# Performance work log

Hardware: AMD Instinct MI355X
Metric: run time of the kernel (lower is better)

## Reference

```python
import jax, jax.numpy as jnp
import numpy as np

D_MODEL = 256
NUM_HEADS = 8
DEPTH = D_MODEL // NUM_HEADS
NEG_BIG = -1e9


def setup_inputs() -> dict:
    key = jax.random.key(0)
    ks = jax.random.split(key, 8)
    B, S = 4, 2048
    inp = {
        "v": jax.random.normal(ks[0], (B, S, D_MODEL), dtype=jnp.float32),
        "k": jax.random.normal(ks[1], (B, S, D_MODEL), dtype=jnp.float32),
        "q": jax.random.normal(ks[2], (B, S, D_MODEL), dtype=jnp.float32),
        "mask": jnp.ones((B, S), dtype=jnp.float32),
        # kernel_size-1 Conv1D without bias == dense projection (d_in, d_out)
        "Wq": jax.random.normal(ks[3], (D_MODEL, D_MODEL), dtype=jnp.float32) * 0.05,
        "Wk": jax.random.normal(ks[4], (D_MODEL, D_MODEL), dtype=jnp.float32) * 0.05,
        "Wv": jax.random.normal(ks[5], (D_MODEL, D_MODEL), dtype=jnp.float32) * 0.05,
        "Wo": jax.random.normal(ks[6], (D_MODEL, D_MODEL), dtype=jnp.float32) * 0.05,
    }
    return inp


def _split_heads(x):
    # (B, S, d_model) -> (B, H, S, depth)
    B, S, _ = x.shape
    return x.reshape(B, S, NUM_HEADS, DEPTH).transpose(0, 2, 1, 3)


def reference(v, k, q, mask, Wq, Wk, Wv, Wo):
    B, S, _ = q.shape
    qh = _split_heads(q @ Wq)  # (B,H,Sq,depth)
    kh = _split_heads(k @ Wk)  # (B,H,Sk,depth)
    vh = _split_heads(v @ Wv)  # (B,H,Sk,depth)

    scale = 1.0 / jnp.sqrt(jnp.asarray(DEPTH, dtype=jnp.float32))
    logits = jnp.einsum("bhqd,bhkd->bhqk", qh, kh) * scale  # (B,H,Sq,Sk)
    mask_att = mask[:, None, None, :]  # broadcast over heads and query dim
    logits = logits + (1.0 - mask_att) * NEG_BIG
    attn = jax.nn.softmax(logits, axis=-1)  # (B,H,Sq,Sk)

    ctx = jnp.einsum("bhqk,bhkd->bhqd", attn, vh)  # (B,H,Sq,depth)
    concat = ctx.transpose(0, 2, 1, 3).reshape(B, S, D_MODEL)
    out = concat @ Wo
    return (out, attn)
```

## Files before the change

kernel.cpp:

```cpp
#include <hip/hip_runtime.h>

#define BB 4
#define HH 8
#define SS 2048
#define DD 32
#define DMODEL 256
#define NEG_BIG_F (-1000000000.0f)
#define SCALE 0.17677669529663687f
#define L2E 1.4426950408889634f
#define SC2 (SCALE * L2E)

typedef short short8 __attribute__((ext_vector_type(8)));
typedef float float4_ __attribute__((ext_vector_type(4)));

__device__ __forceinline__ unsigned short f2bf(float x) {
  unsigned u = __float_as_uint(x);
  u += 0x7FFFu + ((u >> 16) & 1u);
  return (unsigned short)(u >> 16);
}

__global__ __launch_bounds__(256) void prep_w(
    const float* __restrict__ Wq, const float* __restrict__ Wk,
    const float* __restrict__ Wv, const float* __restrict__ Wo,
    unsigned short* __restrict__ wt) {
  __shared__ float tile[32][33];
  int z = blockIdx.z;
  const float* W = (z == 0) ? Wq : (z == 1) ? Wk : (z == 2) ? Wv : Wo;
  unsigned short* dst = wt + (size_t)z * DMODEL * DMODEL;
  int k0 = blockIdx.x * 32, n0 = blockIdx.y * 32;
  int tx = threadIdx.x & 31, ty = threadIdx.x >> 5;
  for (int r = ty; r < 32; r += 8)
    tile[r][tx] = W[(size_t)(k0 + r) * DMODEL + n0 + tx];
  __syncthreads();
  for (int r = ty; r < 32; r += 8)
    dst[(size_t)(n0 + r) * DMODEL + k0 + tx] = f2bf(tile[tx][r]);
}

__global__ __launch_bounds__(256) void proj_kernel(
    const float* __restrict__ q, const float* __restrict__ k,
    const float* __restrict__ v, const unsigned short* __restrict__ wt,
    unsigned short* __restrict__ qh, unsigned short* __restrict__ kh,
    unsigned short* __restrict__ vh) {
  int z = blockIdx.z;
  const float* src = (z == 0) ? q : (z == 1) ? k : v;
  const unsigned short* Wt = wt + (size_t)z * DMODEL * DMODEL;
  unsigned short* dst = (z == 0) ? qh : (z == 1) ? kh : vh;

  int w = threadIdx.x >> 6, lane = threadIdx.x & 63, l16 = lane & 15,
      g = lane >> 4;
  int row = blockIdx.x * 64 + w * 16 + l16;
  int n0 = blockIdx.y * 64;

  float4_ z4 = {0.f, 0.f, 0.f, 0.f};
  float4_ acc[4] = {z4, z4, z4, z4};

  for (int k0 = 0; k0 < DMODEL; k0 += 32) {
    const float4_* ap = (const float4_*)(src + (size_t)row * DMODEL + k0 + 8 * g);
    float4_ a0 = ap[0], a1 = ap[1];
    short8 a;
#pragma unroll
    for (int j = 0; j < 4; ++j) {
      a[j] = (short)f2bf(a0[j]);
      a[4 + j] = (short)f2bf(a1[j]);
    }
#pragma unroll
    for (int cb = 0; cb < 4; ++cb) {
      int n = n0 + cb * 16 + l16;
      short8 bfr = *(const short8*)(Wt + (size_t)n * DMODEL + k0 + 8 * g);
      acc[cb] = __builtin_amdgcn_mfma_f32_16x16x32_bf16(a, bfr, acc[cb], 0, 0, 0);
    }
  }

  int rowbase = blockIdx.x * 64 + w * 16 + 4 * g;
#pragma unroll
  for (int cb = 0; cb < 4; ++cb) {
#pragma unroll
    for (int rr = 0; rr < 4; ++rr) {
      int r = rowbase + rr;
      int c = n0 + cb * 16 + l16;
      int b = r >> 11, s = r & (SS - 1);
      int h = c >> 5, d = c & 31;
      dst[(((size_t)(b * HH + h) * SS + s) * DD) + d] = f2bf(acc[cb][rr]);
    }
  }
}

__global__ __launch_bounds__(256) void fused_attn(
    const unsigned short* __restrict__ qh, const unsigned short* __restrict__ kh,
    const unsigned short* __restrict__ vh, const float* __restrict__ mask,
    float* __restrict__ attn_out, unsigned short* __restrict__ concat) {
  __shared__ float biasl2[SS];
  __shared__ unsigned short vt[32][72];
  __shared__ unsigned short at[4][16][72];

  int bh = blockIdx.y;
  int b = bh >> 3, h = bh & 7;
  for (int i = threadIdx.x; i < SS; i += 256)
    biasl2[i] = (1.0f - mask[(size_t)b * SS + i]) * (NEG_BIG_F * L2E);
  __syncthreads();

  int w = threadIdx.x >> 6, lane = threadIdx.x & 63, l16 = lane & 15,
      g = lane >> 4;
  int q0 = blockIdx.x * 64 + w * 16;

  short8 qa = *(const short8*)(qh + ((size_t)bh * SS + q0 + l16) * DD + 8 * g);

  const unsigned short* kbase = kh + (size_t)bh * SS * DD;
  const unsigned short* vbase = vh + (size_t)bh * SS * DD;
  float4_ z4 = {0.f, 0.f, 0.f, 0.f};

  float m2 = -INFINITY, l = 0.f;
  for (int k0 = 0; k0 < SS; k0 += 32) {
#pragma unroll
    for (int kk = 0; kk < 2; ++kk) {
      int kt = k0 + kk * 16;
      short8 kf = *(const short8*)(kbase + (size_t)(kt + l16) * DD + 8 * g);
      float4_ r = __builtin_amdgcn_mfma_f32_16x16x32_bf16(kf, qa, z4, 0, 0, 0);
      float4_ b4 = *(const float4_*)&biasl2[kt + 4 * g];
      float t0 = fmaf(r[0], SC2, b4[0]);
      float t1 = fmaf(r[1], SC2, b4[1]);
      float t2 = fmaf(r[2], SC2, b4[2]);
      float t3 = fmaf(r[3], SC2, b4[3]);
      float nm = fmaxf(fmaxf(t0, t1), fmaxf(t2, t3));
      nm = fmaxf(nm, m2);
      float s = exp2f(m2 - nm);
      float e = exp2f(t0 - nm) + exp2f(t1 - nm) + exp2f(t2 - nm) +
                exp2f(t3 - nm);
      l = fmaf(l, s, e);
      m2 = nm;
    }
  }
#pragma unroll
  for (int off = 16; off < 64; off <<= 1) {
    float om = __shfl_xor(m2, off);
    float ol = __shfl_xor(l, off);
    float nm = fmaxf(m2, om);
    l = l * exp2f(m2 - nm) + ol * exp2f(om - nm);
    m2 = nm;
  }
  float dq = m2 + log2f(l);

  float* arow = attn_out + (size_t)bh * SS * SS + (size_t)(q0 + l16) * SS;
  float4_ acc0 = z4, acc1 = z4;

  int vr = threadIdx.x >> 2;
  int dseg = (threadIdx.x & 3) * 8;

  for (int kb = 0; kb < SS; kb += 64) {
    __syncthreads();
    {
      short8 vv = *(const short8*)(vbase + (size_t)(kb + vr) * DD + dseg);
#pragma unroll
      for (int j = 0; j < 8; ++j) vt[dseg + j][vr] = (unsigned short)vv[j];
    }
    __syncthreads();

#pragma unroll
    for (int ks = 0; ks < 2; ++ks) {
#pragma unroll
      for (int kt = 0; kt < 2; ++kt) {
        int kk0 = kb + ks * 32 + kt * 16;
        short8 kf = *(const short8*)(kbase + (size_t)(kk0 + l16) * DD + 8 * g);
        float4_ r = __builtin_amdgcn_mfma_f32_16x16x32_bf16(kf, qa, z4, 0, 0, 0);
        float4_ b4 = *(const float4_*)&biasl2[kk0 + 4 * g];
        float4_ p;
#pragma unroll
        for (int rr = 0; rr < 4; ++rr)
          p[rr] = exp2f(fmaf(r[rr], SC2, b4[rr] - dq));
        *(float4_*)(arow + kk0 + 4 * g) = p;
        unsigned u0 = ((unsigned)f2bf(p[1]) << 16) | f2bf(p[0]);
        unsigned u1 = ((unsigned)f2bf(p[3]) << 16) | f2bf(p[2]);
        uint2 pk;
        pk.x = u0;
        pk.y = u1;
        *(uint2*)&at[w][l16][ks * 32 + kt * 16 + 4 * g] = pk;
      }
      short8 pa = *(const short8*)&at[w][l16][ks * 32 + 8 * g];
      short8 b0 = *(const short8*)&vt[l16][ks * 32 + 8 * g];
      short8 b1 = *(const short8*)&vt[16 + l16][ks * 32 + 8 * g];
      acc0 = __builtin_amdgcn_mfma_f32_16x16x32_bf16(pa, b0, acc0, 0, 0, 0);
      acc1 = __builtin_amdgcn_mfma_f32_16x16x32_bf16(pa, b1, acc1, 0, 0, 0);
    }
  }

#pragma unroll
  for (int rr = 0; rr < 4; ++rr) {
    int s = q0 + 4 * g + rr;
    size_t base = ((size_t)b * SS + s) * DMODEL + h * DD;
    concat[base + l16] = f2bf(acc0[rr]);
    concat[base + 16 + l16] = f2bf(acc1[rr]);
  }
}

__global__ __launch_bounds__(256) void outgemm_kernel(
    const unsigned short* __restrict__ concat,
    const unsigned short* __restrict__ wot,
    float* __restrict__ out) {
  int w = threadIdx.x >> 6, lane = threadIdx.x & 63, l16 = lane & 15,
      g = lane >> 4;
  int row = blockIdx.x * 64 + w * 16 + l16;
  int n0 = blockIdx.y * 64;
  float4_ z4 = {0.f, 0.f, 0.f, 0.f};
  float4_ acc[4] = {z4, z4, z4, z4};
  for (int k0 = 0; k0 < DMODEL; k0 += 32) {
    short8 a = *(const short8*)(concat + (size_t)row * DMODEL + k0 + 8 * g);
#pragma unroll
    for (int cb = 0; cb < 4; ++cb) {
      int n = n0 + cb * 16 + l16;
      short8 bfr = *(const short8*)(wot + (size_t)n * DMODEL + k0 + 8 * g);
      acc[cb] = __builtin_amdgcn_mfma_f32_16x16x32_bf16(a, bfr, acc[cb], 0, 0, 0);
    }
  }
  int rowbase = blockIdx.x * 64 + w * 16 + 4 * g;
#pragma unroll
  for (int cb = 0; cb < 4; ++cb)
#pragma unroll
    for (int rr = 0; rr < 4; ++rr)
      out[(size_t)(rowbase + rr) * DMODEL + n0 + cb * 16 + l16] = acc[cb][rr];
}

extern "C" void kernel_launch(void* const* d_in, const int* in_sizes, int n_in,
                              void* d_out, int out_size, void* d_ws,
                              size_t ws_size, hipStream_t stream) {
  const float* v = (const float*)d_in[0];
  const float* k = (const float*)d_in[1];
  const float* q = (const float*)d_in[2];
  const float* mask = (const float*)d_in[3];
  const float* Wq = (const float*)d_in[4];
  const float* Wk = (const float*)d_in[5];
  const float* Wv = (const float*)d_in[6];
  const float* Wo = (const float*)d_in[7];

  float* out = (float*)d_out;
  float* attn = out + (size_t)BB * SS * DMODEL;

  const size_t NH = (size_t)BB * HH * SS * DD;
  unsigned short* qh = (unsigned short*)d_ws;
  unsigned short* kh = qh + NH;
  unsigned short* vh = kh + NH;
  unsigned short* concat = vh + NH;
  unsigned short* wt = concat + (size_t)BB * SS * DMODEL;

  prep_w<<<dim3(8, 8, 4), 256, 0, stream>>>(Wq, Wk, Wv, Wo, wt);
  proj_kernel<<<dim3(128, 4, 3), 256, 0, stream>>>(q, k, v, wt, qh, kh, vh);
  fused_attn<<<dim3(32, 32), 256, 0, stream>>>(qh, kh, vh, mask, attn, concat);
  outgemm_kernel<<<dim3(128, 4), 256, 0, stream>>>(
      concat, wt + (size_t)3 * DMODEL * DMODEL, out);
}
```

Before: 262.7 us.

## Reorder K into MFMA fragment layout, process two query tiles per wave

The projection kernel now writes K in a fragment-ordered layout, so each lane's 16-byte K fragment is contiguous and the attention kernel reads it with one coalesced load per tile. Each wave now handles 32 queries instead of 16, so every loaded K fragment and V tile feeds two MFMA query tiles, and the grid is halved. The first softmax pass drops the running max and only sums exp2 of the biased logits, which removes rescaling work but can overflow if logits grow large. Bf16 packing of probabilities uses the hardware v_cvt_pk_bf16_f32 instruction instead of manual rounding.

```diff
diff --git a/kernel.cpp b/kernel.cpp
--- a/kernel.cpp
+++ b/kernel.cpp
@@ -17,6 +17,12 @@
   unsigned u = __float_as_uint(x);
   u += 0x7FFFu + ((u >> 16) & 1u);
   return (unsigned short)(u >> 16);
+}
+
+__device__ __forceinline__ unsigned cvtpk(float lo, float hi) {
+  unsigned u;
+  asm("v_cvt_pk_bf16_f32 %0, %1, %2" : "=v"(u) : "v"(lo), "v"(hi));
+  return u;
 }
 
 __global__ __launch_bounds__(256) void prep_w(
@@ -39,12 +45,11 @@
 __global__ __launch_bounds__(256) void proj_kernel(
     const float* __restrict__ q, const float* __restrict__ k,
     const float* __restrict__ v, const unsigned short* __restrict__ wt,
-    unsigned short* __restrict__ qh, unsigned short* __restrict__ kh,
+    unsigned short* __restrict__ qh, unsigned short* __restrict__ khf,
     unsigned short* __restrict__ vh) {
   int z = blockIdx.z;
   const float* src = (z == 0) ? q : (z == 1) ? k : v;
   const unsigned short* Wt = wt + (size_t)z * DMODEL * DMODEL;
-  unsigned short* dst = (z == 0) ? qh : (z == 1) ? kh : vh;
 
   int w = threadIdx.x >> 6, lane = threadIdx.x & 63, l16 = lane & 15,
       g = lane >> 4;
@@ -80,18 +85,27 @@
       int c = n0 + cb * 16 + l16;
       int b = r >> 11, s = r & (SS - 1);
       int h = c >> 5, d = c & 31;
-      dst[(((size_t)(b * HH + h) * SS + s) * DD) + d] = f2bf(acc[cb][rr]);
+      int bh = b * HH + h;
+      unsigned short val = f2bf(acc[cb][rr]);
+      if (z == 1) {
+        size_t idx = (((size_t)bh * 128 + (s >> 4)) * 64 +
+                      ((s & 15) + 16 * (d >> 3))) * 8 + (d & 7);
+        khf[idx] = val;
+      } else {
+        unsigned short* dst = (z == 0) ? qh : vh;
+        dst[((size_t)bh * SS + s) * DD + d] = val;
+      }
     }
   }
 }
 
 __global__ __launch_bounds__(256) void fused_attn(
-    const unsigned short* __restrict__ qh, const unsigned short* __restrict__ kh,
+    const unsigned short* __restrict__ qh, const unsigned short* __restrict__ khf,
     const unsigned short* __restrict__ vh, const float* __restrict__ mask,
     float* __restrict__ attn_out, unsigned short* __restrict__ concat) {
   __shared__ float biasl2[SS];
   __shared__ unsigned short vt[32][72];
-  __shared__ unsigned short at[4][16][72];
+  __shared__ unsigned short at[4][32][72];
 
   int bh = blockIdx.y;
   int b = bh >> 3, h = bh & 7;
@@ -101,47 +115,44 @@
 
   int w = threadIdx.x >> 6, lane = threadIdx.x & 63, l16 = lane & 15,
       g = lane >> 4;
-  int q0 = blockIdx.x * 64 + w * 16;
-
-  short8 qa = *(const short8*)(qh + ((size_t)bh * SS + q0 + l16) * DD + 8 * g);
-
-  const unsigned short* kbase = kh + (size_t)bh * SS * DD;
+  int q0 = blockIdx.x * 128 + w * 32;
+
+  short8 qa0 = *(const short8*)(qh + ((size_t)bh * SS + q0 + l16) * DD + 8 * g);
+  short8 qa1 =
+      *(const short8*)(qh + ((size_t)bh * SS + q0 + 16 + l16) * DD + 8 * g);
+
+  const unsigned short* kf_base = khf + ((size_t)bh * 128 * 64 + lane) * 8;
   const unsigned short* vbase = vh + (size_t)bh * SS * DD;
   float4_ z4 = {0.f, 0.f, 0.f, 0.f};
 
-  float m2 = -INFINITY, l = 0.f;
-  for (int k0 = 0; k0 < SS; k0 += 32) {
-#pragma unroll
-    for (int kk = 0; kk < 2; ++kk) {
-      int kt = k0 + kk * 16;
-      short8 kf = *(const short8*)(kbase + (size_t)(kt + l16) * DD + 8 * g);
-      float4_ r = __builtin_amdgcn_mfma_f32_16x16x32_bf16(kf, qa, z4, 0, 0, 0);
-      float4_ b4 = *(const float4_*)&biasl2[kt + 4 * g];
-      float t0 = fmaf(r[0], SC2, b4[0]);
-      float t1 = fmaf(r[1], SC2, b4[1]);
-      float t2 = fmaf(r[2], SC2, b4[2]);
-      float t3 = fmaf(r[3], SC2, b4[3]);
-      float nm = fmaxf(fmaxf(t0, t1), fmaxf(t2, t3));
-      nm = fmaxf(nm, m2);
-      float s = exp2f(m2 - nm);
-      float e = exp2f(t0 - nm) + exp2f(t1 - nm) + exp2f(t2 - nm) +
-                exp2f(t3 - nm);
-      l = fmaf(l, s, e);
-      m2 = nm;
-    }
+  float l0 = 0.f, l1 = 0.f;
+#pragma unroll 4
+  for (int t = 0; t < 128; ++t) {
+    short8 kf = *(const short8*)(kf_base + (size_t)t * 512);
+    float4_ r0 = __builtin_amdgcn_mfma_f32_16x16x32_bf16(kf, qa0, z4, 0, 0, 0);
+    float4_ r1 = __builtin_amdgcn_mfma_f32_16x16x32_bf16(kf, qa1, z4, 0, 0, 0);
+    float4_ b4 = *(const float4_*)&biasl2[t * 16 + 4 * g];
+    float e00 = exp2f(fmaf(r0[0], SC2, b4[0]));
+    float e01 = exp2f(fmaf(r0[1], SC2, b4[1]));
+    float e02 = exp2f(fmaf(r0[2], SC2, b4[2]));
+    float e03 = exp2f(fmaf(r0[3], SC2, b4[3]));
+    l0 += (e00 + e01) + (e02 + e03);
+    float e10 = exp2f(fmaf(r1[0], SC2, b4[0]));
+    float e11 = exp2f(fmaf(r1[1], SC2, b4[1]));
+    float e12 = exp2f(fmaf(r1[2], SC2, b4[2]));
+    float e13 = exp2f(fmaf(r1[3], SC2, b4[3]));
+    l1 += (e10 + e11) + (e12 + e13);
   }
 #pragma unroll
   for (int off = 16; off < 64; off <<= 1) {
-    float om = __shfl_xor(m2, off);
-    float ol = __shfl_xor(l, off);
-    float nm = fmaxf(m2, om);
-    l = l * exp2f(m2 - nm) + ol * exp2f(om - nm);
-    m2 = nm;
-  }
-  float dq = m2 + log2f(l);
-
-  float* arow = attn_out + (size_t)bh * SS * SS + (size_t)(q0 + l16) * SS;
-  float4_ acc0 = z4, acc1 = z4;
+    l0 += __shfl_xor(l0, off);
+    l1 += __shfl_xor(l1, off);
+  }
+  float dq0 = log2f(l0), dq1 = log2f(l1);
+
+  float* arow0 = attn_out + (size_t)bh * SS * SS + (size_t)(q0 + l16) * SS;
+  float* arow1 = arow0 + (size_t)16 * SS;
+  float4_ a00 = z4, a01 = z4, a10 = z4, a11 = z4;
 
   int vr = threadIdx.x >> 2;
   int dseg = (threadIdx.x & 3) * 8;
@@ -159,36 +170,48 @@
     for (int ks = 0; ks < 2; ++ks) {
 #pragma unroll
       for (int kt = 0; kt < 2; ++kt) {
-        int kk0 = kb + ks * 32 + kt * 16;
-        short8 kf = *(const short8*)(kbase + (size_t)(kk0 + l16) * DD + 8 * g);
-        float4_ r = __builtin_amdgcn_mfma_f32_16x16x32_bf16(kf, qa, z4, 0, 0, 0);
-        float4_ b4 = *(const float4_*)&biasl2[kk0 + 4 * g];
-        float4_ p;
-#pragma unroll
-        for (int rr = 0; rr < 4; ++rr)
-          p[rr] = exp2f(fmaf(r[rr], SC2, b4[rr] - dq));
-        *(float4_*)(arow + kk0 + 4 * g) = p;
-        unsigned u0 = ((unsigned)f2bf(p[1]) << 16) | f2bf(p[0]);
-        unsigned u1 = ((unsigned)f2bf(p[3]) << 16) | f2bf(p[2]);
-        uint2 pk;
-        pk.x = u0;
-        pk.y = u1;
-        *(uint2*)&at[w][l16][ks * 32 + kt * 16 + 4 * g] = pk;
+        int t = (kb >> 4) + ks * 2 + kt;
+        int col = ks * 32 + kt * 16 + 4 * g;
+        short8 kf = *(const short8*)(kf_base + (size_t)t * 512);
+        float4_ r0 = __builtin_amdgcn_mfma_f32_16x16x32_bf16(kf, qa0, z4, 0, 0, 0);
+        float4_ r1 = __builtin_amdgcn_mfma_f32_16x16x32_bf16(kf, qa1, z4, 0, 0, 0);
+        float4_ b4 = *(const float4_*)&biasl2[kb + col];
+        float4_ p0, p1;
+#pragma unroll
+        for (int rr = 0; rr < 4; ++rr) {
+          p0[rr] = exp2f(fmaf(r0[rr], SC2, b4[rr] - dq0));
+          p1[rr] = exp2f(fmaf(r1[rr], SC2, b4[rr] - dq1));
+        }
+        *(float4_*)(arow0 + kb + col) = p0;
+        *(float4_*)(arow1 + kb + col) = p1;
+        uint2 pk0, pk1;
+        pk0.x = cvtpk(p0[0], p0[1]);
+        pk0.y = cvtpk(p0[2], p0[3]);
+        pk1.x = cvtpk(p1[0], p1[1]);
+        pk1.y = cvtpk(p1[2], p1[3]);
+        *(uint2*)&at[w][l16][col] = pk0;
+        *(uint2*)&at[w][16 + l16][col] = pk1;
       }
-      short8 pa = *(const short8*)&at[w][l16][ks * 32 + 8 * g];
+      short8 pa0 = *(const short8*)&at[w][l16][ks * 32 + 8 * g];
+      short8 pa1 = *(const short8*)&at[w][16 + l16][ks * 32 + 8 * g];
       short8 b0 = *(const short8*)&vt[l16][ks * 32 + 8 * g];
       short8 b1 = *(const short8*)&vt[16 + l16][ks * 32 + 8 * g];
-      acc0 = __builtin_amdgcn_mfma_f32_16x16x32_bf16(pa, b0, acc0, 0, 0, 0);
-      acc1 = __builtin_amdgcn_mfma_f32_16x16x32_bf16(pa, b1, acc1, 0, 0, 0);
+      a00 = __builtin_amdgcn_mfma_f32_16x16x32_bf16(pa0, b0, a00, 0, 0, 0);
+      a01 = __builtin_amdgcn_mfma_f32_16x16x32_bf16(pa0, b1, a01, 0, 0, 0);
+      a10 = __builtin_amdgcn_mfma_f32_16x16x32_bf16(pa1, b0, a10, 0, 0, 0);
+      a11 = __builtin_amdgcn_mfma_f32_16x16x32_bf16(pa1, b1, a11, 0, 0, 0);
     }
   }
 
 #pragma unroll
   for (int rr = 0; rr < 4; ++rr) {
-    int s = q0 + 4 * g + rr;
-    size_t base = ((size_t)b * SS + s) * DMODEL + h * DD;
-    concat[base + l16] = f2bf(acc0[rr]);
-    concat[base + 16 + l16] = f2bf(acc1[rr]);
+    int s0 = q0 + 4 * g + rr;
+    size_t base0 = ((size_t)b * SS + s0) * DMODEL + h * DD;
+    concat[base0 + l16] = f2bf(a00[rr]);
+    concat[base0 + 16 + l16] = f2bf(a01[rr]);
+    size_t base1 = ((size_t)b * SS + s0 + 16) * DMODEL + h * DD;
+    concat[base1 + l16] = f2bf(a10[rr]);
+    concat[base1 + 16 + l16] = f2bf(a11[rr]);
   }
 }
 
@@ -236,14 +259,14 @@
 
   const size_t NH = (size_t)BB * HH * SS * DD;
   unsigned short* qh = (unsigned short*)d_ws;
-  unsigned short* kh = qh + NH;
-  unsigned short* vh = kh + NH;
+  unsigned short* khf = qh + NH;
+  unsigned short* vh = khf + NH;
   unsigned short* concat = vh + NH;
   unsigned short* wt = concat + (size_t)BB * SS * DMODEL;
 
   prep_w<<<dim3(8, 8, 4), 256, 0, stream>>>(Wq, Wk, Wv, Wo, wt);
-  proj_kernel<<<dim3(128, 4, 3), 256, 0, stream>>>(q, k, v, wt, qh, kh, vh);
-  fused_attn<<<dim3(32, 32), 256, 0, stream>>>(qh, kh, vh, mask, attn, concat);
+  proj_kernel<<<dim3(128, 4, 3), 256, 0, stream>>>(q, k, v, wt, qh, khf, vh);
+  fused_attn<<<dim3(16, 32), 256, 0, stream>>>(qh, khf, vh, mask, attn, concat);
   outgemm_kernel<<<dim3(128, 4), 256, 0, stream>>>(
       concat, wt + (size_t)3 * DMODEL * DMODEL, out);
 }
```

Measured after the change: 342.6 us. 1.3x slower.

## Store V transposed from projection, drop LDS transpose and max-tracking pass

Applied to the files above, without the earlier changes.

The projection kernel now writes V in a per-head transposed (d, s) layout. The attention kernel can then read PV MFMA operands directly from global memory, without the shared-memory transpose and its two barriers per 64-key block. The first softmax pass drops the running-max rescaling and sums plain exp2 of the scaled logits, relying on logits being small enough not to overflow; this removes extra exp2 and max work per key. Bf16 packing of probabilities uses the v_cvt_pk_bf16_f32 instruction instead of manual rounding. The trade-off is that V's transposed global writes are strided, and the missing max subtraction risks overflow for large-magnitude logits.

```diff
diff --git a/kernel.cpp b/kernel.cpp
--- a/kernel.cpp
+++ b/kernel.cpp
@@ -17,6 +17,12 @@
   unsigned u = __float_as_uint(x);
   u += 0x7FFFu + ((u >> 16) & 1u);
   return (unsigned short)(u >> 16);
+}
+
+__device__ __forceinline__ unsigned cvtpk(float lo, float hi) {
+  unsigned u;
+  asm("v_cvt_pk_bf16_f32 %0, %1, %2" : "=v"(u) : "v"(lo), "v"(hi));
+  return u;
 }
 
 __global__ __launch_bounds__(256) void prep_w(
@@ -40,11 +46,10 @@
     const float* __restrict__ q, const float* __restrict__ k,
     const float* __restrict__ v, const unsigned short* __restrict__ wt,
     unsigned short* __restrict__ qh, unsigned short* __restrict__ kh,
-    unsigned short* __restrict__ vh) {
+    unsigned short* __restrict__ vT) {
   int z = blockIdx.z;
   const float* src = (z == 0) ? q : (z == 1) ? k : v;
   const unsigned short* Wt = wt + (size_t)z * DMODEL * DMODEL;
-  unsigned short* dst = (z == 0) ? qh : (z == 1) ? kh : vh;
 
   int w = threadIdx.x >> 6, lane = threadIdx.x & 63, l16 = lane & 15,
       g = lane >> 4;
@@ -80,17 +85,23 @@
       int c = n0 + cb * 16 + l16;
       int b = r >> 11, s = r & (SS - 1);
       int h = c >> 5, d = c & 31;
-      dst[(((size_t)(b * HH + h) * SS + s) * DD) + d] = f2bf(acc[cb][rr]);
+      int bh = b * HH + h;
+      unsigned short val = f2bf(acc[cb][rr]);
+      if (z == 2) {
+        vT[((size_t)bh * DD + d) * SS + s] = val;
+      } else {
+        unsigned short* dst = (z == 0) ? qh : kh;
+        dst[((size_t)bh * SS + s) * DD + d] = val;
+      }
     }
   }
 }
 
 __global__ __launch_bounds__(256) void fused_attn(
     const unsigned short* __restrict__ qh, const unsigned short* __restrict__ kh,
-    const unsigned short* __restrict__ vh, const float* __restrict__ mask,
+    const unsigned short* __restrict__ vT, const float* __restrict__ mask,
     float* __restrict__ attn_out, unsigned short* __restrict__ concat) {
   __shared__ float biasl2[SS];
-  __shared__ unsigned short vt[32][72];
   __shared__ unsigned short at[4][16][72];
 
   int bh = blockIdx.y;
@@ -106,78 +117,53 @@
   short8 qa = *(const short8*)(qh + ((size_t)bh * SS + q0 + l16) * DD + 8 * g);
 
   const unsigned short* kbase = kh + (size_t)bh * SS * DD;
-  const unsigned short* vbase = vh + (size_t)bh * SS * DD;
+  const unsigned short* vtb = vT + (size_t)bh * DD * SS;
   float4_ z4 = {0.f, 0.f, 0.f, 0.f};
 
-  float m2 = -INFINITY, l = 0.f;
-  for (int k0 = 0; k0 < SS; k0 += 32) {
-#pragma unroll
-    for (int kk = 0; kk < 2; ++kk) {
-      int kt = k0 + kk * 16;
-      short8 kf = *(const short8*)(kbase + (size_t)(kt + l16) * DD + 8 * g);
-      float4_ r = __builtin_amdgcn_mfma_f32_16x16x32_bf16(kf, qa, z4, 0, 0, 0);
-      float4_ b4 = *(const float4_*)&biasl2[kt + 4 * g];
-      float t0 = fmaf(r[0], SC2, b4[0]);
-      float t1 = fmaf(r[1], SC2, b4[1]);
-      float t2 = fmaf(r[2], SC2, b4[2]);
-      float t3 = fmaf(r[3], SC2, b4[3]);
-      float nm = fmaxf(fmaxf(t0, t1), fmaxf(t2, t3));
-      nm = fmaxf(nm, m2);
-      float s = exp2f(m2 - nm);
-      float e = exp2f(t0 - nm) + exp2f(t1 - nm) + exp2f(t2 - nm) +
-                exp2f(t3 - nm);
-      l = fmaf(l, s, e);
-      m2 = nm;
-    }
-  }
-#pragma unroll
-  for (int off = 16; off < 64; off <<= 1) {
-    float om = __shfl_xor(m2, off);
-    float ol = __shfl_xor(l, off);
-    float nm = fmaxf(m2, om);
-    l = l * exp2f(m2 - nm) + ol * exp2f(om - nm);
-    m2 = nm;
-  }
-  float dq = m2 + log2f(l);
+  float l = 0.f;
+#pragma unroll 4
+  for (int t = 0; t < 128; ++t) {
+    short8 kf = *(const short8*)(kbase + (size_t)(t * 16 + l16) * DD + 8 * g);
+    float4_ r = __builtin_amdgcn_mfma_f32_16x16x32_bf16(kf, qa, z4, 0, 0, 0);
+    float4_ b4 = *(const float4_*)&biasl2[t * 16 + 4 * g];
+    float e0 = exp2f(fmaf(r[0], SC2, b4[0]));
+    float e1 = exp2f(fmaf(r[1], SC2, b4[1]));
+    float e2 = exp2f(fmaf(r[2], SC2, b4[2]));
+    float e3 = exp2f(fmaf(r[3], SC2, b4[3]));
+    l += (e0 + e1) + (e2 + e3);
+  }
+#pragma unroll
+  for (int off = 16; off < 64; off <<= 1) l += __shfl_xor(l, off);
+  float dq = log2f(l);
 
   float* arow = attn_out + (size_t)bh * SS * SS + (size_t)(q0 + l16) * SS;
   float4_ acc0 = z4, acc1 = z4;
 
-  int vr = threadIdx.x >> 2;
-  int dseg = (threadIdx.x & 3) * 8;
-
   for (int kb = 0; kb < SS; kb += 64) {
-    __syncthreads();
-    {
-      short8 vv = *(const short8*)(vbase + (size_t)(kb + vr) * DD + dseg);
-#pragma unroll
-      for (int j = 0; j < 8; ++j) vt[dseg + j][vr] = (unsigned short)vv[j];
-    }
-    __syncthreads();
-
 #pragma unroll
     for (int ks = 0; ks < 2; ++ks) {
 #pragma unroll
       for (int kt = 0; kt < 2; ++kt) {
-        int kk0 = kb + ks * 32 + kt * 16;
-        short8 kf = *(const short8*)(kbase + (size_t)(kk0 + l16) * DD + 8 * g);
+        int k0 = kb + ks * 32 + kt * 16;
+        int col = ks * 32 + kt * 16 + 4 * g;
+        short8 kf = *(const short8*)(kbase + (size_t)(k0 + l16) * DD + 8 * g);
         float4_ r = __builtin_amdgcn_mfma_f32_16x16x32_bf16(kf, qa, z4, 0, 0, 0);
-        float4_ b4 = *(const float4_*)&biasl2[kk0 + 4 * g];
+        float4_ b4 = *(const float4_*)&biasl2[kb + col];
         float4_ p;
 #pragma unroll
         for (int rr = 0; rr < 4; ++rr)
           p[rr] = exp2f(fmaf(r[rr], SC2, b4[rr] - dq));
-        *(float4_*)(arow + kk0 + 4 * g) = p;
-        unsigned u0 = ((unsigned)f2bf(p[1]) << 16) | f2bf(p[0]);
-        unsigned u1 = ((unsigned)f2bf(p[3]) << 16) | f2bf(p[2]);
+        *(float4_*)(arow + kb + col) = p;
         uint2 pk;
-        pk.x = u0;
-        pk.y = u1;
-        *(uint2*)&at[w][l16][ks * 32 + kt * 16 + 4 * g] = pk;
+        pk.x = cvtpk(p[0], p[1]);
+        pk.y = cvtpk(p[2], p[3]);
+        *(uint2*)&at[w][l16][col] = pk;
       }
       short8 pa = *(const short8*)&at[w][l16][ks * 32 + 8 * g];
-      short8 b0 = *(const short8*)&vt[l16][ks * 32 + 8 * g];
-      short8 b1 = *(const short8*)&vt[16 + l16][ks * 32 + 8 * g];
+      short8 b0 =
+          *(const short8*)(vtb + (size_t)l16 * SS + kb + ks * 32 + 8 * g);
+      short8 b1 =
+          *(const short8*)(vtb + (size_t)(16 + l16) * SS + kb + ks * 32 + 8 * g);
       acc0 = __builtin_amdgcn_mfma_f32_16x16x32_bf16(pa, b0, acc0, 0, 0, 0);
       acc1 = __builtin_amdgcn_mfma_f32_16x16x32_bf16(pa, b1, acc1, 0, 0, 0);
     }
@@ -237,13 +223,13 @@
   const size_t NH = (size_t)BB * HH * SS * DD;
   unsigned short* qh = (unsigned short*)d_ws;
   unsigned short* kh = qh + NH;
-  unsigned short* vh = kh + NH;
-  unsigned short* concat = vh + NH;
+  unsigned short* vT = kh + NH;
+  unsigned short* concat = vT + NH;
   unsigned short* wt = concat + (size_t)BB * SS * DMODEL;
 
   prep_w<<<dim3(8, 8, 4), 256, 0, stream>>>(Wq, Wk, Wv, Wo, wt);
-  proj_kernel<<<dim3(128, 4, 3), 256, 0, stream>>>(q, k, v, wt, qh, kh, vh);
-  fused_attn<<<dim3(32, 32), 256, 0, stream>>>(qh, kh, vh, mask, attn, concat);
+  proj_kernel<<<dim3(128, 4, 3), 256, 0, stream>>>(q, k, v, wt, qh, kh, vT);
+  fused_attn<<<dim3(32, 32), 256, 0, stream>>>(qh, kh, vT, mask, attn, concat);
   outgemm_kernel<<<dim3(128, 4), 256, 0, stream>>>(
       concat, wt + (size_t)3 * DMODEL * DMODEL, out);
 }
```

After: 267.5 us. About the same (+1.8%).
